# Kernel optimization log

Measured on AMD Instinct MI355X. Metric: run time of the kernel, lower is better.

## Reference

```python
import jax, jax.numpy as jnp
import numpy as np

B, C, IMG, P = 32, 3, 224, 16
E, HEADS, L, NC = 768, 8, 6, 1000
HD = E // HEADS            # 96
NP = (IMG // P) ** 2       # 196 patches
N = NP + 1                 # +cls
SCALE = HD ** -0.5
EPS = 1e-5


def layer_norm(x, g, b):
    m = jnp.mean(x, axis=-1, keepdims=True)
    v = jnp.mean(jnp.square(x - m), axis=-1, keepdims=True)
    return (x - m) * jax.lax.rsqrt(v + EPS) * g + b


def _forward(x, conv_w, conv_b, cls_token, pos_emb,
             qkv_w, qkv_b, proj_w, proj_b, ln1_g, ln1_b,
             mlp_w1, mlp_b1, mlp_w2, mlp_b2, ln2_g, ln2_b,
             head_ln_g, head_ln_b, head_w, head_b):
    b = x.shape[0]
    h = IMG // P
    # patch embed: conv with kernel==stride == non-overlapping patch matmul
    xp = x.reshape(b, C, h, P, h, P)                       # b c h i w j
    x = jnp.einsum('bchiwj,ecij->bhwe', xp, conv_w) + conv_b
    x = x.reshape(b, NP, E)
    # cls token + positional embedding (broadcast add, as in torch source)
    cls = jnp.broadcast_to(cls_token[None], (b, 1, E))
    x = jnp.concatenate([cls, x], axis=1) + pos_emb        # [b, N, E]

    def block(x, p):
        qw, qb, pw, pb, g1, b1, w1, bb1, w2, bb2, g2, b2 = p
        # --- attention sublayer (post-norm residual) ---
        qkv = x @ qw.T + qb                                # [b, N, 3E]
        qkv = qkv.reshape(b, N, 3, HEADS, HD)
        qkv = jnp.transpose(qkv, (2, 0, 3, 1, 4))          # [3, b, H, N, d]
        q, k, v = qkv[0], qkv[1], qkv[2]
        sim = jnp.einsum('bhqd,bhkd->bhqk', q, k)
        sim = jax.nn.softmax(sim, axis=-1) * SCALE         # scale AFTER softmax (faithful)
        att = jnp.einsum('bhnk,bhkd->bhnd', sim, v)
        att = jnp.transpose(att, (0, 2, 1, 3)).reshape(b, N, E)
        att = att @ pw.T + pb
        x = layer_norm(x + att, g1, b1)
        # --- MLP sublayer (post-norm residual) ---
        hdn = jax.nn.gelu(x @ w1.T + bb1, approximate=False)
        mlp = hdn @ w2.T + bb2
        x = layer_norm(x + mlp, g2, b2)
        return x, None

    x, _ = jax.lax.scan(block, x, (qkv_w, qkv_b, proj_w, proj_b,
                                   ln1_g, ln1_b, mlp_w1, mlp_b1,
                                   mlp_w2, mlp_b2, ln2_g, ln2_b))
    # classifier: mean pool -> LN -> Linear
    x = jnp.mean(x, axis=1)
    x = layer_norm(x, head_ln_g, head_ln_b)
    return x @ head_w.T + head_b


def setup_inputs() -> dict:
    key = jax.random.key(0)
    ks = jax.random.split(key, 24)
    s = 0.02
    FF = 4 * E
    return {
        'x': jax.random.normal(ks[0], (B, C, IMG, IMG), jnp.float32),
        'conv_w': jax.random.normal(ks[1], (E, C, P, P), jnp.float32) * s,
        'conv_b': jnp.zeros((E,), jnp.float32),
        'cls_token': jax.random.uniform(ks[2], (1, E), jnp.float32),
        'pos_emb': jax.random.uniform(ks[3], (N, E), jnp.float32),
        'qkv_w': jax.random.normal(ks[4], (L, 3 * E, E), jnp.float32) * s,
        'qkv_b': jnp.zeros((L, 3 * E), jnp.float32),
        'proj_w': jax.random.normal(ks[5], (L, E, E), jnp.float32) * s,
        'proj_b': jnp.zeros((L, E), jnp.float32),
        'ln1_g': jnp.ones((L, E), jnp.float32),
        'ln1_b': jnp.zeros((L, E), jnp.float32),
        'mlp_w1': jax.random.normal(ks[6], (L, FF, E), jnp.float32) * s,
        'mlp_b1': jnp.zeros((L, FF), jnp.float32),
        'mlp_w2': jax.random.normal(ks[7], (L, E, FF), jnp.float32) * s,
        'mlp_b2': jnp.zeros((L, E), jnp.float32),
        'ln2_g': jnp.ones((L, E), jnp.float32),
        'ln2_b': jnp.zeros((L, E), jnp.float32),
        'head_ln_g': jnp.ones((E,), jnp.float32),
        'head_ln_b': jnp.zeros((E,), jnp.float32),
        'head_w': jax.random.normal(ks[8], (NC, E), jnp.float32) * s,
        'head_b': jnp.zeros((NC,), jnp.float32),
    }


def reference(x, conv_w, conv_b, cls_token, pos_emb,
              qkv_w, qkv_b, proj_w, proj_b, ln1_g, ln1_b,
              mlp_w1, mlp_b1, mlp_w2, mlp_b2, ln2_g, ln2_b,
              head_ln_g, head_ln_b, head_w, head_b):
    return _forward(x, conv_w, conv_b, cls_token, pos_emb,
                    qkv_w, qkv_b, proj_w, proj_b, ln1_g, ln1_b,
                    mlp_w1, mlp_b1, mlp_w2, mlp_b2, ln2_g, ln2_b,
                    head_ln_g, head_ln_b, head_w, head_b)
```

## Files before the change

### kernel.cpp

```cpp
#include <hip/hip_runtime.h>
#include <hip/hip_bf16.h>
#include <math.h>

constexpr int Bsz = 32, Cch = 3, IMGS = 224, PP = 16;
constexpr int E = 768, HEADS = 8, Lnum = 6, NC = 1000;
constexpr int HD = 96;
constexpr int NP = 196;
constexpr int Nn = 197;
constexpr int FF = 3072;
constexpr float SCALE = 0.10206207261596575f;
constexpr float EPSc  = 1e-5f;

using short8 = __attribute__((ext_vector_type(8))) short;
using f32x4  = __attribute__((ext_vector_type(4))) float;

__device__ __forceinline__ void async_cp16(const void* g, void* l) {
    __builtin_amdgcn_global_load_lds((const __attribute__((address_space(1))) void*)g,
                                     (__attribute__((address_space(3))) void*)l, 16, 0, 0);
}

__global__ void f2b_k(const float* __restrict__ in, __hip_bfloat16* __restrict__ out, int n4) {
    int i = blockIdx.x * 256 + threadIdx.x;
    if (i >= n4) return;
    const float4 v = ((const float4*)in)[i];
    size_t o = (size_t)i * 4;
    out[o + 0] = __float2bfloat16(v.x);
    out[o + 1] = __float2bfloat16(v.y);
    out[o + 2] = __float2bfloat16(v.z);
    out[o + 3] = __float2bfloat16(v.w);
}

__global__ void f2b4_k(const float* __restrict__ s0, const float* __restrict__ s1,
                       const float* __restrict__ s2, const float* __restrict__ s3,
                       __hip_bfloat16* __restrict__ d0, __hip_bfloat16* __restrict__ d1,
                       __hip_bfloat16* __restrict__ d2, __hip_bfloat16* __restrict__ d3,
                       int n0, int n1, int n2, int n3) {
    int i = blockIdx.x * 256 + threadIdx.x;
    const float* s; __hip_bfloat16* d; int base;
    if (i < n0)                { s = s0; d = d0; base = 0; }
    else if (i < n0 + n1)      { s = s1; d = d1; base = n0; }
    else if (i < n0 + n1 + n2) { s = s2; d = d2; base = n0 + n1; }
    else if (i < n0 + n1 + n2 + n3) { s = s3; d = d3; base = n0 + n1 + n2; }
    else return;
    int k = i - base;
    const float4 v = ((const float4*)s)[k];
    size_t o = (size_t)k * 4;
    d[o + 0] = __float2bfloat16(v.x);
    d[o + 1] = __float2bfloat16(v.y);
    d[o + 2] = __float2bfloat16(v.z);
    d[o + 3] = __float2bfloat16(v.w);
}

__global__ void im2col_k(const float* __restrict__ x, __hip_bfloat16* __restrict__ A) {
    int idx = blockIdx.x * 256 + threadIdx.x;
    if (idx >= Bsz * NP * (Cch * PP * PP)) return;
    int col = idx % 768;
    int row = idx / 768;
    int b  = row / NP;
    int p  = row % NP;
    int hh = p / 14, ww = p % 14;
    int c  = col / 256;
    int rem = col % 256;
    int i = rem / 16, j = rem % 16;
    A[idx] = __float2bfloat16(
        x[(((size_t)b * Cch + c) * IMGS + hh * 16 + i) * IMGS + ww * 16 + j]);
}

template <int TM, int OUT_BF16, int ACT, int AHEADS>
__global__ __launch_bounds__(256, 4) void gemm_bf16_k(
    const __hip_bfloat16* __restrict__ A, const __hip_bfloat16* __restrict__ W,
    const float* __restrict__ bias, void* __restrict__ outp,
    int M, int N, int K)
{
    constexpr int NA = TM / 64;
    constexpr int JN = (TM == 128) ? 4 : 2;
    __shared__ char As[TM * 64];
    __shared__ char Bs[8192];
    const int tid  = threadIdx.x;
    const int lane = tid & 63;
    const int w    = tid >> 6;
    const int m0 = blockIdx.x * TM, n0 = blockIdx.y * 128;
    const int wm = (TM == 128) ? (w & 1) * 64 : 0;
    const int wn = (TM == 128) ? (w >> 1) * 64 : w * 32;

    const __hip_bfloat16* agv[NA];
    int abv[NA], acv[NA];
#pragma unroll
    for (int i = 0; i < NA; i++) {
        int q = tid + i * 256;
        int r = q >> 2;
        int c = (q & 3) ^ ((r >> 1) & 3);
        int am = m0 + r; if (am > M - 1) am = M - 1;
        if (AHEADS == 0) {
            agv[i] = A + (size_t)am * K + c * 8;
            abv[i] = 0; acv[i] = 0;
        } else {
            int b_ = am / 197, i_ = am - b_ * 197;
            abv[i] = b_ * 8 * 18912 + i_ * 96;
            acv[i] = c;
            agv[i] = A;
        }
    }
    const int q0 = tid, q1 = tid + 256;
    const int rb0 = q0 >> 2, rb1 = q1 >> 2;
    const int cb0 = (q0 & 3) ^ ((rb0 >> 1) & 3);
    const int cb1 = (q1 & 3) ^ ((rb1 >> 1) & 3);
    const __hip_bfloat16* bg0 = W + (size_t)(n0 + rb0) * K + cb0 * 8;
    const __hip_bfloat16* bg1 = W + (size_t)(n0 + rb1) * K + cb1 * 8;
    char* const asd = As + w * 1024;
    char* const bsd = Bs + w * 1024;

    const int frow = lane & 15, fquad = lane >> 4;
    const int swz = (fquad ^ ((frow >> 1) & 3)) * 16;
    const char* ar = As + (wm + frow) * 64 + swz;
    const char* br = Bs + (wn + frow) * 64 + swz;

    f32x4 acc[4][JN] = {};

#pragma unroll 1
    for (int k0 = 0; k0 < K; k0 += 32) {
#pragma unroll
        for (int i = 0; i < NA; i++) {
            if (AHEADS == 0) {
                async_cp16(agv[i] + k0, asd + i * 4096);
            } else {
                int kc = acv[i] + (k0 >> 3);
                int h = kc / 12, dd = kc - h * 12;
                async_cp16(agv[i] + abv[i] + h * 18912 + dd * 8, asd + i * 4096);
            }
        }
        async_cp16(bg0 + k0, bsd);
        async_cp16(bg1 + k0, bsd + 4096);
        __syncthreads();
        short8 af[4], bf[JN];
#pragma unroll
        for (int i = 0; i < 4; i++) af[i] = *(const short8*)(ar + i * 1024);
#pragma unroll
        for (int j = 0; j < JN; j++) bf[j] = *(const short8*)(br + j * 1024);
#pragma unroll
        for (int i = 0; i < 4; i++)
#pragma unroll
            for (int j = 0; j < JN; j++)
                acc[i][j] = __builtin_amdgcn_mfma_f32_16x16x32_bf16(af[i], bf[j], acc[i][j], 0, 0, 0);
        __syncthreads();
    }

#pragma unroll
    for (int i = 0; i < 4; i++) {
#pragma unroll
        for (int j = 0; j < JN; j++) {
#pragma unroll
            for (int r = 0; r < 4; r++) {
                int row = m0 + wm + i * 16 + fquad * 4 + r;
                int col = n0 + wn + j * 16 + frow;
                if (row < M) {
                    float v = acc[i][j][r] + bias[col];
                    if (ACT == 1) v = 0.5f * v * (1.0f + erff(v * 0.70710678118654752f));
                    if (OUT_BF16) ((__hip_bfloat16*)outp)[(size_t)row * N + col] = __float2bfloat16(v);
                    else          ((float*)outp)[(size_t)row * N + col] = v;
                }
            }
        }
    }
}

__global__ void assemble_k(const float* __restrict__ ptmp, const float* __restrict__ cls,
                           const float* __restrict__ pos, float* __restrict__ X,
                           __hip_bfloat16* __restrict__ Xb) {
    int idx = blockIdx.x * 256 + threadIdx.x;
    if (idx >= Bsz * Nn * E) return;
    int e = idx % E;
    int r = idx / E;
    int n = r % Nn, b = r / Nn;
    float v = (n == 0) ? cls[e] : ptmp[((size_t)b * NP + (n - 1)) * E + e];
    v += pos[(size_t)n * E + e];
    X[idx] = v;
    Xb[idx] = __float2bfloat16(v);
}

__global__ void vtr_k(const __hip_bfloat16* __restrict__ qkv, __hip_bfloat16* __restrict__ Vtg) {
    __shared__ short T[64][104];
    const int tid = threadIdx.x;
    const int bh = blockIdx.y, jc = blockIdx.x;
    const int b = bh >> 3, h = bh & 7;
    const int j0 = jc * 64;
#pragma unroll
    for (int it = 0; it < 3; it++) {
        int idx = it * 256 + tid;
        int jl = idx / 12, off = (idx % 12) * 8;
        int j = j0 + jl;
        short8 v = {0, 0, 0, 0, 0, 0, 0, 0};
        if (j <= 196)
            v = *(const short8*)(qkv + (size_t)(b * Nn + j) * 2304 + 1536 + h * 96 + off);
        *(short8*)(&T[jl][off]) = v;
    }
    __syncthreads();
#pragma unroll
    for (int it = 0; it < 3; it++) {
        int idx = it * 256 + tid;
        int d = idx >> 3, c = idx & 7;
        int col = j0 + c * 8;
        if (col < 232) {
            short8 v;
#pragma unroll
            for (int k = 0; k < 8; k++) v[k] = T[c * 8 + k][d];
            *(short8*)(Vtg + ((size_t)bh * 96 + d) * 232 + col) = v;
        }
    }
}

__global__ __launch_bounds__(256, 1) void fattn_k(
    const __hip_bfloat16* __restrict__ qkv,
    const __hip_bfloat16* __restrict__ Vtg,
    __hip_bfloat16* __restrict__ atth)
{
    __shared__ __align__(16) char SL[44544 + 4 * 1280];
    char* const Ps = SL + 44544;
    const int tid = threadIdx.x, lane = tid & 63, w = tid >> 6;
    const int bh = blockIdx.x;
    const int b = bh >> 3, h = bh & 7;
    const int frow = lane & 15, quad = lane >> 4;

#pragma unroll
    for (int it = 0; it < 10; it++) {
        int c = it * 256 + tid;
        if (c < 197 * 12) {
            int j = c / 12, cc = c % 12;
            short8 v = *(const short8*)(qkv + ((size_t)(b * 197 + j)) * 2304 + 768 + h * 96 + cc * 8);
            *(short8*)(SL + j * 208 + cc * 16) = v;
        }
    }
    __syncthreads();

    short8 pf[4][7];
#pragma unroll 1
    for (int t = 0; t < 4; t++) {
        const int mt = w + 4 * t;
        if (mt >= 13) break;
        const int qi = min(mt * 16 + frow, 196);
        const __hip_bfloat16* qrow = qkv + ((size_t)(b * 197 + qi)) * 2304 + h * 96 + quad * 8;
        short8 qf[3];
#pragma unroll
        for (int kc = 0; kc < 3; kc++) qf[kc] = *(const short8*)(qrow + kc * 32);

        f32x4 sacc[13];
#pragma unroll
        for (int nt = 0; nt < 13; nt++) sacc[nt] = (f32x4){0.f, 0.f, 0.f, 0.f};
#pragma unroll
        for (int nt = 0; nt < 13; nt++) {
#pragma unroll
            for (int kc = 0; kc < 3; kc++) {
                short8 kf = *(const short8*)(SL + (nt * 16 + frow) * 208 + (kc * 32 + quad * 8) * 2);
                sacc[nt] = __builtin_amdgcn_mfma_f32_16x16x32_bf16(qf[kc], kf, sacc[nt], 0, 0, 0);
            }
        }

        float mx[4] = {-1e30f, -1e30f, -1e30f, -1e30f};
#pragma unroll
        for (int nt = 0; nt < 13; nt++) {
            bool masked = (nt == 12) && (frow >= 5);
#pragma unroll
            for (int r = 0; r < 4; r++) {
                float v = masked ? -1e30f : sacc[nt][r];
                sacc[nt][r] = v;
                mx[r] = fmaxf(mx[r], v);
            }
        }
#pragma unroll
        for (int m = 1; m <= 8; m <<= 1)
#pragma unroll
            for (int r = 0; r < 4; r++) mx[r] = fmaxf(mx[r], __shfl_xor(mx[r], m));
        float sm[4] = {0.f, 0.f, 0.f, 0.f};
#pragma unroll
        for (int nt = 0; nt < 13; nt++) {
            bool masked = (nt == 12) && (frow >= 5);
#pragma unroll
            for (int r = 0; r < 4; r++) {
                float e = masked ? 0.f : __expf(sacc[nt][r] - mx[r]);
                sacc[nt][r] = e;
                sm[r] += e;
            }
        }
#pragma unroll
        for (int m = 1; m <= 8; m <<= 1)
#pragma unroll
            for (int r = 0; r < 4; r++) sm[r] += __shfl_xor(sm[r], m);
        float inv[4];
#pragma unroll
        for (int r = 0; r < 4; r++) inv[r] = SCALE / sm[r];

        char* const myPs = Ps + w * 1280;
#pragma unroll
        for (int kc = 0; kc < 7; kc++) {
#pragma unroll
            for (int tt = 0; tt < 2; tt++) {
                int t2 = kc * 2 + tt;
#pragma unroll
                for (int r = 0; r < 4; r++) {
                    float pv = (t2 < 13) ? sacc[t2][r] * inv[r] : 0.f;
                    *(__hip_bfloat16*)(myPs + (quad * 4 + r) * 80 + (tt * 16 + frow) * 2) =
                        __float2bfloat16(pv);
                }
            }
            pf[t][kc] = *(const short8*)(myPs + frow * 80 + quad * 16);
        }
    }
    __syncthreads();

    {
        const char* src = (const char*)(Vtg + (size_t)bh * 96 * 232);
#pragma unroll
        for (int i = 0; i < 11; i++) {
            int c = i * 256 + w * 64 + lane;
            if (c < 96 * 29)
                async_cp16(src + (size_t)c * 16, SL + (size_t)(i * 256 + w * 64) * 16);
        }
    }
    __syncthreads();

#pragma unroll 1
    for (int t = 0; t < 4; t++) {
        const int mt = w + 4 * t;
        if (mt >= 13) break;
        f32x4 oacc[6];
#pragma unroll
        for (int dt = 0; dt < 6; dt++) oacc[dt] = (f32x4){0.f, 0.f, 0.f, 0.f};
#pragma unroll
        for (int kc = 0; kc < 7; kc++) {
#pragma unroll
            for (int dt = 0; dt < 6; dt++) {
                short8 vf = *(const short8*)(SL + (size_t)(dt * 16 + frow) * 464 +
                                             (kc * 32 + quad * 8) * 2);
                oacc[dt] = __builtin_amdgcn_mfma_f32_16x16x32_bf16(pf[t][kc], vf, oacc[dt], 0, 0, 0);
            }
        }
#pragma unroll
        for (int dt = 0; dt < 6; dt++)
#pragma unroll
            for (int r = 0; r < 4; r++) {
                int i = mt * 16 + quad * 4 + r;
                if (i < 197)
                    atth[((size_t)bh * 197 + i) * 96 + dt * 16 + frow] =
                        __float2bfloat16(oacc[dt][r]);
            }
    }
}

__global__ void add_ln_k(float* __restrict__ X, const float* __restrict__ T,
                         const float* __restrict__ g, const float* __restrict__ bb,
                         __hip_bfloat16* __restrict__ Xb) {
    const size_t row = blockIdx.x;
    float* xr = X + row * E;
    const float* tr = T + row * E;
    const int t = threadIdx.x;
    __shared__ float red[4];
    float v[3];
    float s = 0.f;
#pragma unroll
    for (int i = 0; i < 3; i++) {
        v[i] = xr[t + i * 256] + tr[t + i * 256];
        s += v[i];
    }
    for (int off = 32; off > 0; off >>= 1) s += __shfl_down(s, off);
    int wid = t >> 6, lane = t & 63;
    if (lane == 0) red[wid] = s;
    __syncthreads();
    if (t == 0) red[0] = red[0] + red[1] + red[2] + red[3];
    __syncthreads();
    float mean = red[0] / 768.f;
    __syncthreads();
    float s2 = 0.f;
#pragma unroll
    for (int i = 0; i < 3; i++) {
        float dl = v[i] - mean;
        s2 += dl * dl;
    }
    for (int off = 32; off > 0; off >>= 1) s2 += __shfl_down(s2, off);
    if (lane == 0) red[wid] = s2;
    __syncthreads();
    if (t == 0) red[0] = red[0] + red[1] + red[2] + red[3];
    __syncthreads();
    float rs = rsqrtf(red[0] / 768.f + EPSc);
#pragma unroll
    for (int i = 0; i < 3; i++) {
        int e = t + i * 256;
        float o = (v[i] - mean) * rs * g[e] + bb[e];
        xr[e] = o;
        Xb[row * E + e] = __float2bfloat16(o);
    }
}

__global__ void pool_ln_k(const float* __restrict__ X, const float* __restrict__ g,
                          const float* __restrict__ bb, float* __restrict__ pooled) {
    __shared__ float red[4];
    const int b = blockIdx.x, t = threadIdx.x;
    float loc[3];
#pragma unroll
    for (int i = 0; i < 3; i++) {
        int e = t + i * 256;
        float s = 0.f;
        for (int n = 0; n < Nn; n++) s += X[((size_t)(b * Nn + n)) * E + e];
        loc[i] = s / (float)Nn;
    }
    float s = loc[0] + loc[1] + loc[2];
    for (int off = 32; off > 0; off >>= 1) s += __shfl_down(s, off);
    int wid = t >> 6, lane = t & 63;
    if (lane == 0) red[wid] = s;
    __syncthreads();
    if (t == 0) red[0] = red[0] + red[1] + red[2] + red[3];
    __syncthreads();
    float mean = red[0] / 768.f;
    __syncthreads();
    float s2 = 0.f;
#pragma unroll
    for (int i = 0; i < 3; i++) {
        float dl = loc[i] - mean;
        s2 += dl * dl;
    }
    for (int off = 32; off > 0; off >>= 1) s2 += __shfl_down(s2, off);
    if (lane == 0) red[wid] = s2;
    __syncthreads();
    if (t == 0) red[0] = red[0] + red[1] + red[2] + red[3];
    __syncthreads();
    float rs = rsqrtf(red[0] / 768.f + EPSc);
#pragma unroll
    for (int i = 0; i < 3; i++) {
        int e = t + i * 256;
        pooled[(size_t)b * E + e] = (loc[i] - mean) * rs * g[e] + bb[e];
    }
}

__global__ void head_k(const float* __restrict__ pooled, const float* __restrict__ hw,
                       const float* __restrict__ hb, float* __restrict__ out) {
    __shared__ float ps[768];
    const int b = blockIdx.y;
    const int s = blockIdx.x;
    const int t = threadIdx.x, lane = t & 63, w = t >> 6;
    for (int e = t; e < 768; e += 256) ps[e] = pooled[(size_t)b * E + e];
    __syncthreads();
    float pl[12];
#pragma unroll
    for (int j = 0; j < 12; j++) pl[j] = ps[j * 64 + lane];
    for (int i = 0; i < 10; i++) {
        int o = s * 40 + w * 10 + i;
        const float* wr = hw + (size_t)o * 768;
        float acc = 0.f;
#pragma unroll
        for (int j = 0; j < 12; j++) acc += pl[j] * wr[j * 64 + lane];
        for (int off = 32; off > 0; off >>= 1) acc += __shfl_down(acc, off);
        if (lane == 0) out[(size_t)b * NC + o] = acc + hb[o];
    }
}

extern "C" void kernel_launch(void* const* d_in, const int* in_sizes, int n_in,
                              void* d_out, int out_size, void* d_ws, size_t ws_size,
                              hipStream_t stream) {
    const float* x        = (const float*)d_in[0];
    const float* conv_w   = (const float*)d_in[1];
    const float* conv_b   = (const float*)d_in[2];
    const float* cls_tok  = (const float*)d_in[3];
    const float* pos_emb  = (const float*)d_in[4];
    const float* qkv_w    = (const float*)d_in[5];
    const float* qkv_b    = (const float*)d_in[6];
    const float* proj_w   = (const float*)d_in[7];
    const float* proj_b   = (const float*)d_in[8];
    const float* ln1_g    = (const float*)d_in[9];
    const float* ln1_b    = (const float*)d_in[10];
    const float* mlp_w1   = (const float*)d_in[11];
    const float* mlp_b1   = (const float*)d_in[12];
    const float* mlp_w2   = (const float*)d_in[13];
    const float* mlp_b2   = (const float*)d_in[14];
    const float* ln2_g    = (const float*)d_in[15];
    const float* ln2_b    = (const float*)d_in[16];
    const float* hln_g    = (const float*)d_in[17];
    const float* hln_b    = (const float*)d_in[18];
    const float* head_w   = (const float*)d_in[19];
    const float* head_b   = (const float*)d_in[20];
    float* out = (float*)d_out;

    const int M = Bsz * Nn;

    char* p = (char*)d_ws;
    __hip_bfloat16* Xb   = (__hip_bfloat16*)p;  p += (size_t)M * E * 2;
    float*          X    = (float*)p;           p += (size_t)M * E * 4;
    __hip_bfloat16* qwb  = (__hip_bfloat16*)p;  p += (size_t)3 * E * E * 2;
    __hip_bfloat16* pwb  = (__hip_bfloat16*)p;  p += (size_t)E * E * 2;
    __hip_bfloat16* w1b  = (__hip_bfloat16*)p;  p += (size_t)FF * E * 2;
    __hip_bfloat16* w2b  = (__hip_bfloat16*)p;  p += (size_t)E * FF * 2;
    __hip_bfloat16* cwb  = (__hip_bfloat16*)p;  p += (size_t)E * E * 2;
    __hip_bfloat16* atth = (__hip_bfloat16*)p;  p += (size_t)M * E * 2;
    float*          pool = (float*)p;           p += (size_t)Bsz * E * 4;
    char* R = p;
    __hip_bfloat16* qkvb = (__hip_bfloat16*)R;
    __hip_bfloat16* Vtg  = (__hip_bfloat16*)(R + 29048832);
    __hip_bfloat16* Hb   = (__hip_bfloat16*)R;
    float*          Ctmp = (float*)(R + 40452096);
    __hip_bfloat16* imb  = (__hip_bfloat16*)R;

    {
        f2b_k<<<(E * E / 4 + 255) / 256, 256, 0, stream>>>(conv_w, cwb, E * E / 4);
        int tot = Bsz * NP * 768;
        im2col_k<<<(tot + 255) / 256, 256, 0, stream>>>(x, imb);
        dim3 g(98, 6);
        gemm_bf16_k<64, 0, 0, 0><<<g, 256, 0, stream>>>(imb, cwb, conv_b, Ctmp, Bsz * NP, E, E);
        int tot2 = Bsz * Nn * E;
        assemble_k<<<(tot2 + 255) / 256, 256, 0, stream>>>(Ctmp, cls_tok, pos_emb, X, Xb);
    }

    const int MB128 = (M + 127) / 128;
    const int MB64  = (M + 63) / 64;
    const int cn0 = 3 * E * E / 4, cn1 = E * E / 4, cn2 = FF * E / 4, cn3 = E * FF / 4;
    const int cgrid = (cn0 + cn1 + cn2 + cn3 + 255) / 256;

    for (int l = 0; l < Lnum; l++) {
        const float* qw = qkv_w + (size_t)l * 3 * E * E;
        const float* qb = qkv_b + (size_t)l * 3 * E;
        const float* pw = proj_w + (size_t)l * E * E;
        const float* pb = proj_b + (size_t)l * E;
        const float* g1 = ln1_g + (size_t)l * E;
        const float* b1 = ln1_b + (size_t)l * E;
        const float* w1 = mlp_w1 + (size_t)l * FF * E;
        const float* bb1 = mlp_b1 + (size_t)l * FF;
        const float* w2 = mlp_w2 + (size_t)l * E * FF;
        const float* bb2 = mlp_b2 + (size_t)l * E;
        const float* g2 = ln2_g + (size_t)l * E;
        const float* b2 = ln2_b + (size_t)l * E;

        f2b4_k<<<cgrid, 256, 0, stream>>>(qw, pw, w1, w2, qwb, pwb, w1b, w2b,
                                          cn0, cn1, cn2, cn3);

        gemm_bf16_k<128, 1, 0, 0><<<dim3(MB128, 18), 256, 0, stream>>>(Xb, qwb, qb, qkvb, M, 3 * E, E);
        vtr_k<<<dim3(4, Bsz * HEADS), 256, 0, stream>>>(qkvb, Vtg);
        fattn_k<<<Bsz * HEADS, 256, 0, stream>>>(qkvb, Vtg, atth);
        gemm_bf16_k<64, 0, 0, 1><<<dim3(MB64, 6), 256, 0, stream>>>(atth, pwb, pb, Ctmp, M, E, E);
        add_ln_k<<<M, 256, 0, stream>>>(X, Ctmp, g1, b1, Xb);
        gemm_bf16_k<128, 1, 1, 0><<<dim3(MB128, 24), 256, 0, stream>>>(Xb, w1b, bb1, Hb, M, FF, E);
        gemm_bf16_k<64, 0, 0, 0><<<dim3(MB64, 6), 256, 0, stream>>>(Hb, w2b, bb2, Ctmp, M, E, FF);
        add_ln_k<<<M, 256, 0, stream>>>(X, Ctmp, g2, b2, Xb);
    }

    pool_ln_k<<<Bsz, 256, 0, stream>>>(X, hln_g, hln_b, pool);
    head_k<<<dim3(25, Bsz), 256, 0, stream>>>(pool, head_w, head_b, out);
}
```

Before: 1.983 ms.

## Double-buffer GEMM LDS tiles and remap blocks across XCDs

The bf16 GEMM now keeps two LDS buffers for A and B and issues the next k-tile's async global-to-LDS loads before computing on the current one. Partial vmcnt waits and explicit barriers let loads overlap with MFMA work. Block indices are also remapped so that consecutive tiles land on the same XCD, which is meant to improve L2 reuse. In exchange, LDS use per block doubles, which may reduce occupancy, and the loop assumes an even number of k iterations.

```diff
diff --git a/kernel.cpp b/kernel.cpp
--- a/kernel.cpp
+++ b/kernel.cpp
@@ -74,12 +74,21 @@
 {
     constexpr int NA = TM / 64;
     constexpr int JN = (TM == 128) ? 4 : 2;
-    __shared__ char As[TM * 64];
-    __shared__ char Bs[8192];
+    __shared__ char As[2][TM * 64];
+    __shared__ char Bs[2][8192];
     const int tid  = threadIdx.x;
     const int lane = tid & 63;
     const int w    = tid >> 6;
-    const int m0 = blockIdx.x * TM, n0 = blockIdx.y * 128;
+
+    const int GX = (int)gridDim.x, GY = (int)gridDim.y;
+    const int nb  = GX * GY;
+    const int lin = (int)blockIdx.x + GX * (int)blockIdx.y;
+    const int qq  = nb >> 3, rr = nb & 7;
+    const int xcd = lin & 7, j8 = lin >> 3;
+    const int s   = (xcd < rr ? xcd * (qq + 1) : rr * (qq + 1) + (xcd - rr) * qq) + j8;
+    const int bx  = s / GY;
+    const int by  = s - bx * GY;
+    const int m0 = bx * TM, n0 = by * 128;
     const int wm = (TM == 128) ? (w & 1) * 64 : 0;
     const int wn = (TM == 128) ? (w >> 1) * 64 : w * 32;
 
@@ -107,43 +116,87 @@
     const int cb1 = (q1 & 3) ^ ((rb1 >> 1) & 3);
     const __hip_bfloat16* bg0 = W + (size_t)(n0 + rb0) * K + cb0 * 8;
     const __hip_bfloat16* bg1 = W + (size_t)(n0 + rb1) * K + cb1 * 8;
-    char* const asd = As + w * 1024;
-    char* const bsd = Bs + w * 1024;
+    char* const asd0 = As[0] + w * 1024;
+    char* const asd1 = As[1] + w * 1024;
+    char* const bsd0 = Bs[0] + w * 1024;
+    char* const bsd1 = Bs[1] + w * 1024;
 
     const int frow = lane & 15, fquad = lane >> 4;
     const int swz = (fquad ^ ((frow >> 1) & 3)) * 16;
-    const char* ar = As + (wm + frow) * 64 + swz;
-    const char* br = Bs + (wn + frow) * 64 + swz;
+    const char* const ar0 = As[0] + (wm + frow) * 64 + swz;
+    const char* const ar1 = As[1] + (wm + frow) * 64 + swz;
+    const char* const br0 = Bs[0] + (wn + frow) * 64 + swz;
+    const char* const br1 = Bs[1] + (wn + frow) * 64 + swz;
 
     f32x4 acc[4][JN] = {};
 
+#define STAGE(k0_, asd_, bsd_)                                                \
+    {                                                                         \
+        _Pragma("unroll")                                                     \
+        for (int i_ = 0; i_ < NA; i_++) {                                     \
+            if (AHEADS == 0) {                                                \
+                async_cp16(agv[i_] + (k0_), (asd_) + i_ * 4096);              \
+            } else {                                                          \
+                int kc_ = acv[i_] + ((k0_) >> 3);                             \
+                int h_ = kc_ / 12, dd_ = kc_ - h_ * 12;                       \
+                async_cp16(agv[i_] + abv[i_] + h_ * 18912 + dd_ * 8,          \
+                           (asd_) + i_ * 4096);                               \
+            }                                                                 \
+        }                                                                     \
+        async_cp16(bg0 + (k0_), (bsd_));                                      \
+        async_cp16(bg1 + (k0_), (bsd_) + 4096);                               \
+    }
+
+#define WAIT_N()                                                              \
+    {                                                                         \
+        if constexpr (TM == 128) asm volatile("s_waitcnt vmcnt(4)" ::: "memory"); \
+        else                     asm volatile("s_waitcnt vmcnt(3)" ::: "memory"); \
+    }
+
+#define FENCE_BAR()                                                           \
+    {                                                                         \
+        __builtin_amdgcn_sched_barrier(0);                                    \
+        __builtin_amdgcn_s_barrier();                                         \
+        __builtin_amdgcn_sched_barrier(0);                                    \
+    }
+
+#define COMPUTE(arp_, brp_)                                                   \
+    {                                                                         \
+        short8 af[4], bf[JN];                                                 \
+        _Pragma("unroll")                                                     \
+        for (int i_ = 0; i_ < 4; i_++) af[i_] = *(const short8*)((arp_) + i_ * 1024); \
+        _Pragma("unroll")                                                     \
+        for (int j_ = 0; j_ < JN; j_++) bf[j_] = *(const short8*)((brp_) + j_ * 1024); \
+        _Pragma("unroll")                                                     \
+        for (int i_ = 0; i_ < 4; i_++)                                        \
+            _Pragma("unroll")                                                 \
+            for (int j_ = 0; j_ < JN; j_++)                                   \
+                acc[i_][j_] = __builtin_amdgcn_mfma_f32_16x16x32_bf16(af[i_], bf[j_], acc[i_][j_], 0, 0, 0); \
+    }
+
+    const int kiters = K / 32;
+    STAGE(0, asd0, bsd0);
 #pragma unroll 1
-    for (int k0 = 0; k0 < K; k0 += 32) {
-#pragma unroll
-        for (int i = 0; i < NA; i++) {
-            if (AHEADS == 0) {
-                async_cp16(agv[i] + k0, asd + i * 4096);
-            } else {
-                int kc = acv[i] + (k0 >> 3);
-                int h = kc / 12, dd = kc - h * 12;
-                async_cp16(agv[i] + abv[i] + h * 18912 + dd * 8, asd + i * 4096);
-            }
-        }
-        async_cp16(bg0 + k0, bsd);
-        async_cp16(bg1 + k0, bsd + 4096);
-        __syncthreads();
-        short8 af[4], bf[JN];
-#pragma unroll
-        for (int i = 0; i < 4; i++) af[i] = *(const short8*)(ar + i * 1024);
-#pragma unroll
-        for (int j = 0; j < JN; j++) bf[j] = *(const short8*)(br + j * 1024);
-#pragma unroll
-        for (int i = 0; i < 4; i++)
-#pragma unroll
-            for (int j = 0; j < JN; j++)
-                acc[i][j] = __builtin_amdgcn_mfma_f32_16x16x32_bf16(af[i], bf[j], acc[i][j], 0, 0, 0);
-        __syncthreads();
-    }
+    for (int it = 0; it < kiters; it += 2) {
+        STAGE((it + 1) * 32, asd1, bsd1);
+        WAIT_N();
+        FENCE_BAR();
+        COMPUTE(ar0, br0);
+        FENCE_BAR();
+        if (it + 2 < kiters) {
+            STAGE((it + 2) * 32, asd0, bsd0);
+            WAIT_N();
+        } else {
+            asm volatile("s_waitcnt vmcnt(0)" ::: "memory");
+        }
+        FENCE_BAR();
+        COMPUTE(ar1, br1);
+        if (it + 2 < kiters) FENCE_BAR();
+    }
+#undef STAGE
+#undef WAIT_N
+#undef FENCE_BAR
+#undef COMPUTE
 
 #pragma unroll
     for (int i = 0; i < 4; i++) {
```

After: 1.898 ms. 1.04x faster.
